# Performance work log

Measured on AMD Instinct MI355X. Metric: run time of the kernel, lower is better.

## Reference

```python
import jax, jax.numpy as jnp
import numpy as np
from jax import lax

RATIOS = (0.5, 1.0, 2.0)
SCALES = (8, 16, 32)
BASE = 16
STRIDE = 16
N_PRE = 6000
N_POST = 300      # post-NMS proposals kept
NMS_THRESH = 0.7
MIN_SIZE = 16.0


def _anchor_base():
    x = y = BASE / 2.0
    ab = np.zeros((len(RATIOS) * len(SCALES), 4), np.float32)
    for i, r in enumerate(RATIOS):
        for j, s in enumerate(SCALES):
            h = BASE * s * np.sqrt(r)
            w = BASE * s * np.sqrt(1.0 / r)
            k = i * len(SCALES) + j
            ab[k] = [y - h / 2, x - w / 2, y + h / 2, x + w / 2]
    return ab


def _anchors(h, w):
    ab = _anchor_base()
    sy = np.arange(0, h * STRIDE, STRIDE)
    sx = np.arange(0, w * STRIDE, STRIDE)
    sx, sy = np.meshgrid(sx, sy)
    shift = np.stack((sy.ravel(), sx.ravel(), sy.ravel(), sx.ravel()), axis=1)
    # [K, A, 4] -> [K*A, 4], row-major over (y, x) pixels matching NHWC flatten
    return (ab[None, :, :] + shift[:, None, :]).reshape(-1, 4).astype(np.float32)


def _conv(x, w, b, pad):
    y = lax.conv_general_dilated(x, w, (1, 1), ((pad, pad), (pad, pad)),
                                 dimension_numbers=('NCHW', 'OIHW', 'NCHW'))
    return y + b[None, :, None, None]


def _loc2bbox(anchor, loc):
    h = anchor[:, 2] - anchor[:, 0]
    w = anchor[:, 3] - anchor[:, 1]
    cy = anchor[:, 0] + 0.5 * h
    cx = anchor[:, 1] + 0.5 * w
    dy, dx, dh, dw = loc[:, 0], loc[:, 1], loc[:, 2], loc[:, 3]
    ncy = dy * h + cy
    ncx = dx * w + cx
    nh = jnp.exp(dh) * h
    nw = jnp.exp(dw) * w
    return jnp.stack([ncy - 0.5 * nh, ncx - 0.5 * nw, ncy + 0.5 * nh, ncx + 0.5 * nw], axis=1)


def _iou(b):
    tl = jnp.maximum(b[:, None, :2], b[None, :, :2])
    br = jnp.minimum(b[:, None, 2:], b[None, :, 2:])
    wh = jnp.clip(br - tl, 0.0)
    inter = wh[..., 0] * wh[..., 1]
    area = (b[:, 2] - b[:, 0]) * (b[:, 3] - b[:, 1])
    return inter / (area[:, None] + area[None, :] - inter + 1e-9)


def _nms_keep(iou):
    # greedy NMS over score-sorted boxes: suppress later boxes overlapping kept earlier ones
    n = iou.shape[0]
    idx = jnp.arange(n)
    def step(keep, i):
        sup = (iou[i] > NMS_THRESH) & (idx > i) & keep[i]
        return keep & (~sup), None
    keep, _ = lax.scan(step, jnp.ones((n,), dtype=bool), idx)
    return keep


def _proposal(loc, fg, anchor, img_h, img_w, scale=1.0):
    boxes = _loc2bbox(anchor, loc)
    boxes = jnp.stack([jnp.clip(boxes[:, 0], 0.0, img_h),
                       jnp.clip(boxes[:, 1], 0.0, img_w),
                       jnp.clip(boxes[:, 2], 0.0, img_h),
                       jnp.clip(boxes[:, 3], 0.0, img_w)], axis=1)
    hs = boxes[:, 2] - boxes[:, 0]
    ws = boxes[:, 3] - boxes[:, 1]
    ms = MIN_SIZE * scale
    score = jnp.where((hs >= ms) & (ws >= ms), fg, -jnp.inf)
    top, idx = lax.top_k(score, N_PRE)
    bk = boxes[idx]                                    # [N_PRE, 4]
    keep = _nms_keep(_iou(lax.stop_gradient(bk)))      # selection is non-differentiable
    fs = jnp.where(keep, top, -jnp.inf)
    _, o2 = lax.top_k(fs, N_POST)
    return bk[o2]                                      # [N_POST, 4]


def setup_inputs() -> dict:
    key = jax.random.key(0)
    ks = jax.random.split(key, 4)
    C, H, W = 512, 50, 76
    return {
        "feature": jax.random.normal(ks[0], (1, C, H, W), jnp.float32),
        "conv1_w": jax.random.normal(ks[1], (512, C, 3, 3), jnp.float32) * 0.01,
        "conv1_b": jnp.zeros((512,), jnp.float32),
        "score_w": jax.random.normal(ks[2], (18, 512, 1, 1), jnp.float32) * 0.01,
        "score_b": jnp.zeros((18,), jnp.float32),
        "loc_w": jax.random.normal(ks[3], (36, 512, 1, 1), jnp.float32) * 0.01,
        "loc_b": jnp.zeros((36,), jnp.float32),
        "img_h": 800,
        "img_w": 1216,
    }


def reference(feature, conv1_w, conv1_b, score_w, score_b, loc_w, loc_b, img_h, img_w):
    _, c, h, w = feature.shape
    A = 9
    anchor = jnp.asarray(_anchors(h, w))
    x = jax.nn.relu(_conv(feature, conv1_w, conv1_b, 1))
    locs = _conv(x, loc_w, loc_b, 0)
    rpn_locs = locs.transpose(0, 2, 3, 1).reshape(1, -1, 4)
    sc = _conv(x, score_w, score_b, 0).transpose(0, 2, 3, 1)   # [1, h, w, 2A]
    sm = jax.nn.softmax(sc.reshape(1, h, w, A, 2), axis=-1)
    fg = sm[..., 1].reshape(-1)
    rpn_scores = sc.reshape(1, -1, 2)
    rois = _proposal(rpn_locs[0], fg, anchor, float(img_h), float(img_w), scale=1.0)
    return rpn_locs, rpn_scores, rois, anchor
```

## Files before the change

### kernel.cpp

```cpp
#include <hip/hip_runtime.h>

#define HH 50
#define WW2 76
#define NPIX 3800
#define CIN 512
#define NANCH 34200
#define NPRE 6000
#define NPOST 300
#define WPR 94

typedef unsigned long long u64;
typedef unsigned int u32;

__device__ __forceinline__ int PADL(int i) { return i + (i >> 4); }

template <bool DOW>
__global__ __launch_bounds__(256) void rpn_wtrans(const float* __restrict__ wgt,
                                                  float* __restrict__ wt,
                                                  const float* __restrict__ sw,
                                                  const float* __restrict__ lw,
                                                  float* __restrict__ wt2,
                                                  u32* __restrict__ hist,
                                                  u32* __restrict__ info) {
    __shared__ float tile[32][33];
    const int bx = blockIdx.x;
    const int by = blockIdx.y;
    const int t  = threadIdx.x;
    const int tx = t & 31, ty = t >> 5;
    int gid = (by * 144 + bx) * 256 + t;
    if (gid < 65536) hist[gid] = 0u;
    else if (gid < 65552) info[gid - 65536] = 0u;
    if (gid < 32768) {
        int c = gid >> 6, n = gid & 63;
        float v = 0.f;
        if (n < 18) v = sw[n * 512 + c];
        else if (n < 54) v = lw[(n - 18) * 512 + c];
        wt2[((c >> 2) * 64 + n) * 4 + (c & 3)] = v;
    }
    if (!DOW) return;
#pragma unroll
    for (int r = 0; r < 32; r += 8) {
        int ko = by * 32 + ty + r;
        tile[ty + r][tx] = wgt[(size_t)ko * 4608 + bx * 32 + tx];
    }
    __syncthreads();
#pragma unroll
    for (int r = 0; r < 32; r += 8) {
        int cit = bx * 32 + ty + r;
        wt[(size_t)cit * 512 + by * 32 + tx] = tile[tx][ty + r];
    }
}

template <bool USEWT>
__global__ __launch_bounds__(256, 4) void rpn_conv1(
    const float* __restrict__ feat, const float* __restrict__ wsrc,
    float* __restrict__ Xp, int cin_blk) {
    const int yb = blockIdx.x;
    const int kg = blockIdx.y;
    const int cz = blockIdx.z;
    const int t  = threadIdx.x;
    const int kp = t & 31;
    const int ty = t >> 5;
    const int row  = ty >> 2;
    const int xseg = ty & 3;
    const int x0 = xseg * 20;
    __shared__ float in_l[1408];
    __shared__ float w_l[2304];

    const int y0 = yb * 2 - 1;
    int inSrc[6]; u32 inValid = 0, inPad = 0;
#pragma unroll
    for (int k = 0; k < 6; ++k) {
        int q = t + k * 256;
        int c = q / 336, rem = q - c * 336;
        int r = rem / 84, xx = rem - r * 84;
        int gy = y0 + r, gx = xx - 1;
        bool inb = q < 1344;
        bool ok = inb && ((unsigned)gy < 50u) && ((unsigned)gx < 76u);
        inSrc[k] = c * NPIX + gy * 76 + gx;
        if (ok) inValid |= (1u << k);
        else if (inb) inPad |= (1u << k);
    }
#pragma unroll
    for (int k = 0; k < 6; ++k)
        if ((inPad >> k) & 1) in_l[t + k * 256] = 0.f;

    const float* wb;
    int wOffA = 0;
    int wSrc[9];
    if (USEWT) {
        wb = wsrc + (size_t)(cz * cin_blk) * 9 * 512 + kg * 64;
        wOffA = 8 * t - 7 * (t & 63);
    } else {
        wb = wsrc + (size_t)(kg * 64) * 4608 + (size_t)(cz * cin_blk) * 9;
#pragma unroll
        for (int k = 0; k < 9; ++k) {
            int q = t + k * 256;
            int c = q / 576, r2 = q - c * 576;
            int tap = r2 >> 6, ko = r2 & 63;
            wSrc[k] = ko * 4608 + c * 9 + tap;
        }
    }

    const float* fb = feat + (size_t)(cz * cin_blk) * NPIX;
    float acc0[20], acc1[20];
#pragma unroll
    for (int p = 0; p < 20; ++p) { acc0[p] = 0.f; acc1[p] = 0.f; }

    const int niter = cin_blk >> 2;
#pragma unroll 1
    for (int it = 0; it < niter; ++it) {
        __syncthreads();
#pragma unroll
        for (int k = 0; k < 6; ++k)
            if ((inValid >> k) & 1) in_l[t + k * 256] = fb[inSrc[k]];
        if (USEWT) {
#pragma unroll
            for (int k = 0; k < 9; ++k)
                w_l[t + k * 256] = wb[wOffA + k * 2048];
        } else {
#pragma unroll
            for (int k = 0; k < 9; ++k)
                w_l[t + k * 256] = wb[wSrc[k]];
        }
        __syncthreads();
#pragma unroll 1
        for (int c = 0; c < 4; ++c) {
            const float* ir0 = &in_l[(c * 4 + row) * 84 + x0];
            const float* wl  = &w_l[c * 576 + 2 * kp];
#pragma unroll
            for (int r = 0; r < 3; ++r) {
                const float* ir = ir0 + r * 84;
                float win[22];
#pragma unroll
                for (int w = 0; w < 22; ++w) win[w] = ir[w];
                float w00 = wl[(r * 3 + 0) * 64],     w01 = wl[(r * 3 + 1) * 64],     w02 = wl[(r * 3 + 2) * 64];
                float w10 = wl[(r * 3 + 0) * 64 + 1], w11 = wl[(r * 3 + 1) * 64 + 1], w12 = wl[(r * 3 + 2) * 64 + 1];
#pragma unroll
                for (int p = 0; p < 20; ++p) {
                    acc0[p] = fmaf(w00, win[p],     acc0[p]);
                    acc0[p] = fmaf(w01, win[p + 1], acc0[p]);
                    acc0[p] = fmaf(w02, win[p + 2], acc0[p]);
                    acc1[p] = fmaf(w10, win[p],     acc1[p]);
                    acc1[p] = fmaf(w11, win[p + 1], acc1[p]);
                    acc1[p] = fmaf(w12, win[p + 2], acc1[p]);
                }
            }
        }
        fb += 4 * NPIX;
        wb += USEWT ? 4 * 9 * 512 : 36;
    }

    const int k0 = kg * 64 + 2 * kp;
    const int y = yb * 2 + row;
    float* d0 = Xp + ((size_t)cz * 512 + k0) * NPIX + y * 76 + x0;
#pragma unroll
    for (int p = 0; p < 20; p += 2) {
        if (x0 + p + 1 < 76) {
            *reinterpret_cast<float2*>(d0 + p)        = make_float2(acc0[p], acc0[p + 1]);
            *reinterpret_cast<float2*>(d0 + NPIX + p) = make_float2(acc1[p], acc1[p + 1]);
        }
    }
}

__global__ __launch_bounds__(256) void rpn_combine(
    const float* __restrict__ Xp, const float* __restrict__ bias,
    float* __restrict__ Xt, int nz) {
    const int p0 = blockIdx.x * 256;
    const int c0 = blockIdx.y * 16;
    const int t  = threadIdx.x;
    __shared__ float s[16][257];
    const int p = p0 + t;
#pragma unroll 4
    for (int i = 0; i < 16; ++i) {
        float v = 0.f;
        if (p < NPIX) {
            size_t base = (size_t)(c0 + i) * NPIX + p;
            float a = bias[c0 + i];
            for (int z = 0; z < nz; ++z) a += Xp[(size_t)z * 512 * NPIX + base];
            v = fmaxf(a, 0.f);
        }
        s[i][t] = v;
    }
    __syncthreads();
    const int cs = (t & 3) * 4;
    const int pr = t >> 2;
#pragma unroll
    for (int q = 0; q < 4; ++q) {
        int p2 = p0 + pr + q * 64;
        if (p2 < NPIX) {
            int pi = pr + q * 64;
            float4 v = make_float4(s[cs][pi], s[cs + 1][pi], s[cs + 2][pi], s[cs + 3][pi]);
            *reinterpret_cast<float4*>(&Xt[(size_t)p2 * 512 + c0 + cs]) = v;
        }
    }
}

__global__ __launch_bounds__(64) void rpn_head(
    const float* __restrict__ Xt, const float* __restrict__ wt2,
    const float* __restrict__ sb, const float* __restrict__ lb,
    const int* __restrict__ ihp, const int* __restrict__ iwp,
    float* __restrict__ out, float* __restrict__ boxes,
    u32* __restrict__ keys, u32* __restrict__ hist) {
    const int p0 = blockIdx.x * 8;
    const int t  = threadIdx.x;
    __shared__ __align__(16) float xs[8 * 512];
    __shared__ float ovl[8][64];
    const float4* src = reinterpret_cast<const float4*>(Xt + (size_t)p0 * 512);
    float4* dst = reinterpret_cast<float4*>(xs);
#pragma unroll
    for (int i = 0; i < 16; ++i) dst[t + i * 64] = src[t + i * 64];
    __syncthreads();
    float acc[8];
    {
        float b = (t < 18) ? sb[t] : ((t < 54) ? lb[t - 18] : 0.f);
#pragma unroll
        for (int px = 0; px < 8; ++px) acc[px] = b;
    }
    const float4* wv = reinterpret_cast<const float4*>(wt2) + t;
#pragma unroll 4
    for (int c4 = 0; c4 < 128; ++c4) {
        float4 w = wv[c4 * 64];
#pragma unroll
        for (int px = 0; px < 8; ++px) {
            float4 x = *reinterpret_cast<const float4*>(xs + px * 512 + c4 * 4);
            acc[px] = fmaf(w.x, x.x, acc[px]);
            acc[px] = fmaf(w.y, x.y, acc[px]);
            acc[px] = fmaf(w.z, x.z, acc[px]);
            acc[px] = fmaf(w.w, x.w, acc[px]);
        }
    }
#pragma unroll
    for (int px = 0; px < 8; ++px) ovl[px][t] = acc[px];
    __syncthreads();
    const float ch = (float)(*ihp), cw = (float)(*iwp);
#pragma unroll
    for (int pass = 0; pass < 2; ++pass) {
        int a, px;
        bool act;
        if (pass == 0) { act = (t < 63); px = t / 9; a = t - px * 9; }
        else           { act = (t < 9);  px = 7;     a = t; }
        if (act) {
            const int p = p0 + px;
            const float* ov = ovl[px];
            const float s0 = ov[2 * a], s1 = ov[2 * a + 1];
            const float dy = ov[18 + 4 * a], dx = ov[18 + 4 * a + 1];
            const float dh = ov[18 + 4 * a + 2], dw = ov[18 + 4 * a + 3];
            const int yy = p / WW2, xx = p % WW2;
            const int ai = p * 9 + a;
            *reinterpret_cast<float4*>(out + ai * 4) = make_float4(dy, dx, dh, dw);
            *reinterpret_cast<float2*>(out + 136800 + ai * 2) = make_float2(s0, s1);
            double r  = (a < 3) ? 0.5 : (a < 6) ? 1.0 : 2.0;
            int m3 = a % 3;
            double s2 = (m3 == 0) ? 8.0 : (m3 == 1) ? 16.0 : 32.0;
            double hd = (16.0 * s2) * sqrt(r);
            double wd = (16.0 * s2) * sqrt(1.0 / r);
            float ay1 = (float)(8.0 - hd * 0.5), ax1 = (float)(8.0 - wd * 0.5);
            float ay2 = (float)(8.0 + hd * 0.5), ax2 = (float)(8.0 + wd * 0.5);
            float fy = (float)(yy * 16), fx = (float)(xx * 16);
            float A0 = ay1 + fy, A1 = ax1 + fx, A2 = ay2 + fy, A3 = ax2 + fx;
            *reinterpret_cast<float4*>(out + 206400 + ai * 4) = make_float4(A0, A1, A2, A3);
            float ah = __fsub_rn(A2, A0), aw = __fsub_rn(A3, A1);
            float cy = __fadd_rn(A0, __fmul_rn(0.5f, ah));
            float cx = __fadd_rn(A1, __fmul_rn(0.5f, aw));
            float ncy = __fadd_rn(__fmul_rn(dy, ah), cy);
            float ncx = __fadd_rn(__fmul_rn(dx, aw), cx);
            float nh = __fmul_rn(expf(dh), ah);
            float nw = __fmul_rn(expf(dw), aw);
            float b0 = __fsub_rn(ncy, __fmul_rn(0.5f, nh));
            float b1 = __fsub_rn(ncx, __fmul_rn(0.5f, nw));
            float b2 = __fadd_rn(ncy, __fmul_rn(0.5f, nh));
            float b3 = __fadd_rn(ncx, __fmul_rn(0.5f, nw));
            b0 = fminf(fmaxf(b0, 0.f), ch); b2 = fminf(fmaxf(b2, 0.f), ch);
            b1 = fminf(fmaxf(b1, 0.f), cw); b3 = fminf(fmaxf(b3, 0.f), cw);
            float hs = __fsub_rn(b2, b0), wsz = __fsub_rn(b3, b1);
            float m = fmaxf(s0, s1);
            float e0 = expf(__fsub_rn(s0, m)), e1 = expf(__fsub_rn(s1, m));
            float fg = __fdiv_rn(e1, __fadd_rn(e0, e1));
            float score = (hs >= 16.f && wsz >= 16.f) ? fg : -__builtin_inff();
            *reinterpret_cast<float4*>(boxes + ai * 4) = make_float4(b0, b1, b2, b3);
            u32 kb = __float_as_uint(score);
            kb = (kb & 0x80000000u) ? ~kb : (kb | 0x80000000u);
            keys[ai] = kb;
            atomicAdd(&hist[kb >> 16], 1u);
        }
    }
}

__global__ __launch_bounds__(1024) void rpn_topk(const u32* __restrict__ hist,
                                                 const u32* __restrict__ keys,
                                                 const float* __restrict__ boxes,
                                                 float* __restrict__ bk) {
    __shared__ u64 s[8704];
    __shared__ u32 part[256], h2[256];
    __shared__ int segs;
    __shared__ u32 Tsh, cnt;
    const int t = threadIdx.x;
    if (t == 0) cnt = 0u;
    u32* tmp = (u32*)s;
    {
        u32 sum = 0;
        const u32* hp = hist + t * 64;
#pragma unroll 8
        for (int b = 0; b < 64; ++b) sum += hp[b];
        tmp[t] = sum;
    }
    __syncthreads();
    u32 p4 = 0;
    if (t < 256) p4 = tmp[4 * t] + tmp[4 * t + 1] + tmp[4 * t + 2] + tmp[4 * t + 3];
    __syncthreads();
    if (t < 256) part[t] = p4;
    __syncthreads();
    for (int off = 1; off < 256; off <<= 1) {
        u32 v = 0, add = 0;
        if (t < 256) { v = part[t]; add = (t + off < 256) ? part[t + off] : 0u; }
        __syncthreads();
        if (t < 256) part[t] = v + add;
        __syncthreads();
    }
    if (t < 256) {
        u32 suf  = part[t];
        u32 sufn = (t < 255) ? part[t + 1] : 0u;
        if (suf >= NPRE && sufn < NPRE) segs = t;
    }
    __syncthreads();
    const int seg = segs;
    const u32 above = (seg < 255) ? part[seg + 1] : 0u;
    if (t < 256) h2[t] = hist[seg * 256 + t];
    __syncthreads();
    for (int off = 1; off < 256; off <<= 1) {
        u32 v = 0, add = 0;
        if (t < 256) { v = h2[t]; add = (t + off < 256) ? h2[t + off] : 0u; }
        __syncthreads();
        if (t < 256) h2[t] = v + add;
        __syncthreads();
    }
    if (t < 256) {
        u32 tot  = above + h2[t];
        u32 totn = above + ((t < 255) ? h2[t + 1] : 0u);
        if (tot >= NPRE && totn < NPRE) Tsh = (u32)(seg * 256 + t);
    }
    __syncthreads();
    const u32 T = Tsh;
    const int lane = t & 63;
    for (int base = 0; base < NANCH; base += 1024) {
        int idx = base + t;
        u32 k = (idx < NANCH) ? keys[idx] : 0u;
        bool sel = (idx < NANCH) && ((k >> 16) >= T);
        u64 ball = __ballot(sel);
        u32 wbase = 0;
        if (lane == 0 && ball) wbase = atomicAdd(&cnt, (u32)__popcll(ball));
        wbase = __shfl(wbase, 0);
        if (sel) {
            u32 pos = wbase + (u32)__popcll(ball & ((1ull << lane) - 1ull));
            if (pos < 8192) s[PADL((int)pos)] = ((u64)k << 32) | (u64)(0xFFFFFFFFu - (u32)idx);
        }
    }
    __syncthreads();
    {
        int n = (int)cnt; if (n > 8192) n = 8192;
        for (int i = t; i < 8192; i += 1024)
            if (i >= n) s[PADL(i)] = 0ull;
    }
    __syncthreads();
    for (int k = 2; k <= 8192; k <<= 1) {
        for (int j = k >> 1; j > 0; j >>= 1) {
#pragma unroll 4
            for (int z = 0; z < 4; ++z) {
                int pi = t + z * 1024;
                int p1 = ((pi & ~(j - 1)) << 1) | (pi & (j - 1));
                int p2 = p1 | j;
                bool desc = ((p1 & k) == 0);
                u64 A = s[PADL(p1)], B = s[PADL(p2)];
                if (desc ? (A < B) : (A > B)) { s[PADL(p1)] = B; s[PADL(p2)] = A; }
            }
            __syncthreads();
        }
    }
    for (int i = t; i < NPRE; i += 1024) {
        u32 oi = 0xFFFFFFFFu - (u32)(s[PADL(i)] & 0xFFFFFFFFull);
        if (oi >= NANCH) oi = 0;
        reinterpret_cast<float4*>(bk)[i] = reinterpret_cast<const float4*>(boxes)[oi];
    }
}

__global__ __launch_bounds__(64) void rpn_iou(const float* __restrict__ bk,
                                              u64* __restrict__ mask) {
    const int t = threadIdx.x;
    const int bj = blockIdx.x, bi = blockIdx.y;
    const int j0 = bj * 64;
    const int i = bi * 64 + t;
    if (j0 + 63 <= bi * 64) {
        if (i < NPRE) mask[(size_t)i * WPR + bj] = 0ull;
        return;
    }
    __shared__ float4 jb[64];
    jb[t] = (j0 + t < NPRE) ? reinterpret_cast<const float4*>(bk)[j0 + t]
                            : make_float4(0.f, 0.f, 0.f, 0.f);
    __syncthreads();
    if (i >= NPRE) return;
    float4 b = reinterpret_cast<const float4*>(bk)[i];
    float areai = __fmul_rn(__fsub_rn(b.z, b.x), __fsub_rn(b.w, b.y));
    u64 bits = 0ull;
    for (int jj = 0; jj < 64; ++jj) {
        int j = j0 + jj;
        if (j <= i || j >= NPRE) continue;
        float4 c = jb[jj];
        float ty = fmaxf(b.x, c.x), tx = fmaxf(b.y, c.y);
        float by = fminf(b.z, c.z), bx2 = fminf(b.w, c.w);
        float ih = fmaxf(__fsub_rn(by, ty), 0.f);
        float iw = fmaxf(__fsub_rn(bx2, tx), 0.f);
        float inter = __fmul_rn(ih, iw);
        float areaj = __fmul_rn(__fsub_rn(c.z, c.x), __fsub_rn(c.w, c.y));
        float denom = __fadd_rn(__fsub_rn(__fadd_rn(areai, areaj), inter), 1e-9f);
        float iou = __fdiv_rn(inter, denom);
        if (iou > 0.7f) bits |= (1ull << jj);
    }
    mask[(size_t)i * WPR + bj] = bits;
}

__global__ __launch_bounds__(64) void rpn_nms(const u64* __restrict__ mask,
                                              const float* __restrict__ bk,
                                              float* __restrict__ rois) {
    const int lane = threadIdx.x;
    u64 rem0 = 0ull, rem1 = 0ull, curW = 0ull;
    __shared__ unsigned short klist[304];
    int kcnt = 0;
    u64 pm0[16], pm1[16], pmg[16];
#pragma unroll
    for (int u = 0; u < 16; ++u) {
        pm0[u] = mask[(size_t)u * WPR + lane];
        pm1[u] = (lane < 30) ? mask[(size_t)u * WPR + 64 + lane] : 0ull;
        pmg[u] = mask[(size_t)u * WPR + 0];
    }
    bool done = false;
    for (int base = 0; base < NPRE && !done; base += 16) {
        if ((base & 63) == 0) {
            int w = base >> 6;
            curW = (w < 64) ? __shfl(rem0, w) : __shfl(rem1, w - 64);
        }
#pragma unroll
        for (int u = 0; u < 16; ++u) {
            const int i = base + u;
            u64 m0 = pm0[u], m1 = pm1[u], mg = pmg[u];
            const int ni = i + 16;
            pm0[u] = mask[(size_t)ni * WPR + lane];
            pm1[u] = (lane < 30) ? mask[(size_t)ni * WPR + 64 + lane] : 0ull;
            pmg[u] = mask[(size_t)ni * WPR + (ni >> 6)];
            if (((curW >> (i & 63)) & 1ull) == 0ull) {
                rem0 |= m0;
                rem1 |= m1;
                curW |= mg;
                if (lane == 0 && kcnt < 304) klist[kcnt] = (unsigned short)i;
                ++kcnt;
                if (kcnt >= NPOST) { done = true; break; }
            }
        }
    }
    __syncthreads();
    const int nk = kcnt < NPOST ? kcnt : NPOST;
    for (int r = lane; r < nk; r += 64) {
        int bi = klist[r];
        reinterpret_cast<float4*>(rois)[r] = reinterpret_cast<const float4*>(bk)[bi];
    }
    if (kcnt < NPOST) {
        int pos = kcnt;
        for (int i = 0; i < NPRE && pos < NPOST; ++i) {
            int w = i >> 6;
            u64 wv = (w < 64) ? __shfl(rem0, w) : __shfl(rem1, w - 64);
            if ((wv >> (i & 63)) & 1ull) {
                if (lane < 4) rois[pos * 4 + lane] = bk[i * 4 + lane];
                ++pos;
            }
        }
    }
}

extern "C" void kernel_launch(void* const* d_in, const int* in_sizes, int n_in,
                              void* d_out, int out_size, void* d_ws, size_t ws_size,
                              hipStream_t stream) {
    (void)in_sizes; (void)n_in; (void)out_size;
    const float* feat = (const float*)d_in[0];
    const float* w1   = (const float*)d_in[1];
    const float* b1   = (const float*)d_in[2];
    const float* sw   = (const float*)d_in[3];
    const float* sb   = (const float*)d_in[4];
    const float* lw   = (const float*)d_in[5];
    const float* lb   = (const float*)d_in[6];
    const int*   ih   = (const int*)d_in[7];
    const int*   iw   = (const int*)d_in[8];
    float* out = (float*)d_out;

    const size_t WT_B    = 9437184;
    const size_t WT2_B   = 131072;
    const size_t XT_B    = 7782400;
    const size_t REST_B  = WT2_B + 547200 + 136800 + 262144 + 64 + 96000 + 4528128;
    const size_t SLICE_B = (size_t)512 * NPIX * 4;
    int nz; bool usewt;
    if      (ws_size >= 8 * SLICE_B + WT_B + XT_B + REST_B) { nz = 8; usewt = true; }
    else if (ws_size >= 4 * SLICE_B + WT_B + XT_B + REST_B) { nz = 4; usewt = true; }
    else if (ws_size >= 2 * SLICE_B + WT_B + XT_B + REST_B) { nz = 2; usewt = true; }
    else                                                    { nz = 2; usewt = false; }

    char* p = (char*)d_ws;
    float* Xp = (float*)p;           p += (size_t)nz * SLICE_B;
    float* wt = nullptr;
    if (usewt) { wt = (float*)p;     p += WT_B; }
    float* Xt     = (float*)p;       p += XT_B;
    float* wt2    = (float*)p;       p += WT2_B;
    float* boxes  = (float*)p;       p += 547200;
    u32*   keys   = (u32*)p;         p += 136800;
    u32*   hist   = (u32*)p;         p += 262144;
    u32*   info   = (u32*)p;         p += 64;
    float* bk     = (float*)p;       p += 96000;
    u64*   mask   = (u64*)p;

    const int cin_blk = 512 / nz;

    if (usewt) {
        rpn_wtrans<true><<<dim3(144, 16), 256, 0, stream>>>(w1, wt, sw, lw, wt2, hist, info);
        rpn_conv1<true><<<dim3(25, 8, nz), 256, 0, stream>>>(feat, wt, Xp, cin_blk);
    } else {
        rpn_wtrans<false><<<dim3(144, 16), 256, 0, stream>>>(w1, nullptr, sw, lw, wt2, hist, info);
        rpn_conv1<false><<<dim3(25, 8, nz), 256, 0, stream>>>(feat, w1, Xp, cin_blk);
    }
    rpn_combine<<<dim3(15, 32), 256, 0, stream>>>(Xp, b1, Xt, nz);
    rpn_head<<<475, 64, 0, stream>>>(Xt, wt2, sb, lb, ih, iw, out, boxes, keys, hist);
    rpn_topk<<<1, 1024, 0, stream>>>(hist, keys, boxes, bk);
    rpn_iou<<<dim3(WPR, WPR), 64, 0, stream>>>(bk, mask);
    rpn_nms<<<1, 64, 0, stream>>>(mask, bk, out + 205200);
}
```

Before: 656.4 us.

## Retile conv1 to 4 outputs x 4 rows, write NHWC, fuse combine into head

The conv1 kernel now computes 4 output channels per thread over 4 output rows per block (19-pixel segments), which raises register reuse of the input window across more channels. Partial results are written directly in pixel-major (NHWC) layout with float4 stores. The separate combine kernel is removed, and the split-K partial sums plus bias and ReLU are now reduced inside the head kernel as it loads its tile. This saves one launch and one full intermediate round trip, at the cost of higher register pressure (occupancy hint lowered to 2) and strided per-thread output stores.

Measured after the change: 623.9 us. 5.0% less time.

```diff
diff --git a/kernel.cpp b/kernel.cpp
--- a/kernel.cpp
+++ b/kernel.cpp
@@ -52,37 +52,37 @@
 }
 
 template <bool USEWT>
-__global__ __launch_bounds__(256, 4) void rpn_conv1(
+__global__ __launch_bounds__(256, 2) void rpn_conv1(
     const float* __restrict__ feat, const float* __restrict__ wsrc,
-    float* __restrict__ Xp, int cin_blk) {
+    float* __restrict__ Xpt, int cin_blk) {
     const int yb = blockIdx.x;
     const int kg = blockIdx.y;
     const int cz = blockIdx.z;
     const int t  = threadIdx.x;
-    const int kp = t & 31;
-    const int ty = t >> 5;
+    const int kp = t & 15;
+    const int ty = t >> 4;
     const int row  = ty >> 2;
     const int xseg = ty & 3;
-    const int x0 = xseg * 20;
-    __shared__ float in_l[1408];
+    const int x0 = xseg * 19;
+    __shared__ float in_l[2048];
     __shared__ float w_l[2304];
 
-    const int y0 = yb * 2 - 1;
-    int inSrc[6]; u32 inValid = 0, inPad = 0;
-#pragma unroll
-    for (int k = 0; k < 6; ++k) {
+    const int y0 = yb * 4 - 1;
+    int inSrc[8]; u32 inValid = 0, inPad = 0;
+#pragma unroll
+    for (int k = 0; k < 8; ++k) {
         int q = t + k * 256;
-        int c = q / 336, rem = q - c * 336;
+        int c = q / 504, rem = q - c * 504;
         int r = rem / 84, xx = rem - r * 84;
         int gy = y0 + r, gx = xx - 1;
-        bool inb = q < 1344;
+        bool inb = q < 2016;
         bool ok = inb && ((unsigned)gy < 50u) && ((unsigned)gx < 76u);
         inSrc[k] = c * NPIX + gy * 76 + gx;
         if (ok) inValid |= (1u << k);
         else if (inb) inPad |= (1u << k);
     }
 #pragma unroll
-    for (int k = 0; k < 6; ++k)
+    for (int k = 0; k < 8; ++k)
         if ((inPad >> k) & 1) in_l[t + k * 256] = 0.f;
 
     const float* wb;
@@ -103,16 +103,18 @@
     }
 
     const float* fb = feat + (size_t)(cz * cin_blk) * NPIX;
-    float acc0[20], acc1[20];
-#pragma unroll
-    for (int p = 0; p < 20; ++p) { acc0[p] = 0.f; acc1[p] = 0.f; }
+    float acc[4][19];
+#pragma unroll
+    for (int o = 0; o < 4; ++o)
+#pragma unroll
+        for (int p = 0; p < 19; ++p) acc[o][p] = 0.f;
 
     const int niter = cin_blk >> 2;
 #pragma unroll 1
     for (int it = 0; it < niter; ++it) {
         __syncthreads();
 #pragma unroll
-        for (int k = 0; k < 6; ++k)
+        for (int k = 0; k < 8; ++k)
             if ((inValid >> k) & 1) in_l[t + k * 256] = fb[inSrc[k]];
         if (USEWT) {
 #pragma unroll
@@ -126,24 +128,29 @@
         __syncthreads();
 #pragma unroll 1
         for (int c = 0; c < 4; ++c) {
-            const float* ir0 = &in_l[(c * 4 + row) * 84 + x0];
-            const float* wl  = &w_l[c * 576 + 2 * kp];
+            const float* ir0 = &in_l[(c * 6 + row) * 84 + x0];
+            const float* wl  = &w_l[c * 576 + 4 * kp];
 #pragma unroll
             for (int r = 0; r < 3; ++r) {
                 const float* ir = ir0 + r * 84;
-                float win[22];
-#pragma unroll
-                for (int w = 0; w < 22; ++w) win[w] = ir[w];
-                float w00 = wl[(r * 3 + 0) * 64],     w01 = wl[(r * 3 + 1) * 64],     w02 = wl[(r * 3 + 2) * 64];
-                float w10 = wl[(r * 3 + 0) * 64 + 1], w11 = wl[(r * 3 + 1) * 64 + 1], w12 = wl[(r * 3 + 2) * 64 + 1];
-#pragma unroll
-                for (int p = 0; p < 20; ++p) {
-                    acc0[p] = fmaf(w00, win[p],     acc0[p]);
-                    acc0[p] = fmaf(w01, win[p + 1], acc0[p]);
-                    acc0[p] = fmaf(w02, win[p + 2], acc0[p]);
-                    acc1[p] = fmaf(w10, win[p],     acc1[p]);
-                    acc1[p] = fmaf(w11, win[p + 1], acc1[p]);
-                    acc1[p] = fmaf(w12, win[p + 2], acc1[p]);
+                float win[21];
+#pragma unroll
+                for (int w = 0; w < 21; ++w) win[w] = ir[w];
+                float wv[4][3];
+#pragma unroll
+                for (int tp = 0; tp < 3; ++tp) {
+                    const float* wr = wl + (r * 3 + tp) * 64;
+#pragma unroll
+                    for (int o = 0; o < 4; ++o) wv[o][tp] = wr[o];
+                }
+#pragma unroll
+                for (int p = 0; p < 19; ++p) {
+#pragma unroll
+                    for (int o = 0; o < 4; ++o) {
+                        acc[o][p] = fmaf(wv[o][0], win[p],     acc[o][p]);
+                        acc[o][p] = fmaf(wv[o][1], win[p + 1], acc[o][p]);
+                        acc[o][p] = fmaf(wv[o][2], win[p + 2], acc[o][p]);
+                    }
                 }
             }
         }
@@ -151,65 +158,43 @@
         wb += USEWT ? 4 * 9 * 512 : 36;
     }
 
-    const int k0 = kg * 64 + 2 * kp;
-    const int y = yb * 2 + row;
-    float* d0 = Xp + ((size_t)cz * 512 + k0) * NPIX + y * 76 + x0;
-#pragma unroll
-    for (int p = 0; p < 20; p += 2) {
-        if (x0 + p + 1 < 76) {
-            *reinterpret_cast<float2*>(d0 + p)        = make_float2(acc0[p], acc0[p + 1]);
-            *reinterpret_cast<float2*>(d0 + NPIX + p) = make_float2(acc1[p], acc1[p + 1]);
-        }
-    }
-}
-
-__global__ __launch_bounds__(256) void rpn_combine(
-    const float* __restrict__ Xp, const float* __restrict__ bias,
-    float* __restrict__ Xt, int nz) {
-    const int p0 = blockIdx.x * 256;
-    const int c0 = blockIdx.y * 16;
-    const int t  = threadIdx.x;
-    __shared__ float s[16][257];
-    const int p = p0 + t;
-#pragma unroll 4
-    for (int i = 0; i < 16; ++i) {
-        float v = 0.f;
-        if (p < NPIX) {
-            size_t base = (size_t)(c0 + i) * NPIX + p;
-            float a = bias[c0 + i];
-            for (int z = 0; z < nz; ++z) a += Xp[(size_t)z * 512 * NPIX + base];
-            v = fmaxf(a, 0.f);
-        }
-        s[i][t] = v;
-    }
-    __syncthreads();
-    const int cs = (t & 3) * 4;
-    const int pr = t >> 2;
-#pragma unroll
-    for (int q = 0; q < 4; ++q) {
-        int p2 = p0 + pr + q * 64;
-        if (p2 < NPIX) {
-            int pi = pr + q * 64;
-            float4 v = make_float4(s[cs][pi], s[cs + 1][pi], s[cs + 2][pi], s[cs + 3][pi]);
-            *reinterpret_cast<float4*>(&Xt[(size_t)p2 * 512 + c0 + cs]) = v;
-        }
+    const int k0 = kg * 64 + 4 * kp;
+    const int y = yb * 4 + row;
+    if (y < 50) {
+        float* d0 = Xpt + ((size_t)cz * NPIX + y * 76 + x0) * 512 + k0;
+#pragma unroll
+        for (int p = 0; p < 19; ++p)
+            *reinterpret_cast<float4*>(d0 + (size_t)p * 512) =
+                make_float4(acc[0][p], acc[1][p], acc[2][p], acc[3][p]);
     }
 }
 
 __global__ __launch_bounds__(64) void rpn_head(
-    const float* __restrict__ Xt, const float* __restrict__ wt2,
+    const float* __restrict__ Xpt, const float* __restrict__ wt2,
+    const float* __restrict__ b1,
     const float* __restrict__ sb, const float* __restrict__ lb,
     const int* __restrict__ ihp, const int* __restrict__ iwp,
     float* __restrict__ out, float* __restrict__ boxes,
-    u32* __restrict__ keys, u32* __restrict__ hist) {
+    u32* __restrict__ keys, u32* __restrict__ hist, int nz) {
     const int p0 = blockIdx.x * 8;
     const int t  = threadIdx.x;
     __shared__ __align__(16) float xs[8 * 512];
     __shared__ float ovl[8][64];
-    const float4* src = reinterpret_cast<const float4*>(Xt + (size_t)p0 * 512);
     float4* dst = reinterpret_cast<float4*>(xs);
 #pragma unroll
-    for (int i = 0; i < 16; ++i) dst[t + i * 64] = src[t + i * 64];
+    for (int i = 0; i < 16; ++i) {
+        int idx = t + i * 64;
+        int px = idx >> 7, cc = idx & 127;
+        float4 v = *reinterpret_cast<const float4*>(b1 + cc * 4);
+        const float* src = Xpt + ((size_t)(p0 + px)) * 512 + cc * 4;
+        for (int z = 0; z < nz; ++z) {
+            float4 x = *reinterpret_cast<const float4*>(src + (size_t)z * NPIX * 512);
+            v.x += x.x; v.y += x.y; v.z += x.z; v.w += x.w;
+        }
+        v.x = fmaxf(v.x, 0.f); v.y = fmaxf(v.y, 0.f);
+        v.z = fmaxf(v.z, 0.f); v.w = fmaxf(v.w, 0.f);
+        dst[idx] = v;
+    }
     __syncthreads();
     float acc[8];
     {
@@ -268,17 +253,17 @@
             float nh = __fmul_rn(expf(dh), ah);
             float nw = __fmul_rn(expf(dw), aw);
             float b0 = __fsub_rn(ncy, __fmul_rn(0.5f, nh));
-            float b1 = __fsub_rn(ncx, __fmul_rn(0.5f, nw));
+            float b1v = __fsub_rn(ncx, __fmul_rn(0.5f, nw));
             float b2 = __fadd_rn(ncy, __fmul_rn(0.5f, nh));
             float b3 = __fadd_rn(ncx, __fmul_rn(0.5f, nw));
             b0 = fminf(fmaxf(b0, 0.f), ch); b2 = fminf(fmaxf(b2, 0.f), ch);
-            b1 = fminf(fmaxf(b1, 0.f), cw); b3 = fminf(fmaxf(b3, 0.f), cw);
-            float hs = __fsub_rn(b2, b0), wsz = __fsub_rn(b3, b1);
+            b1v = fminf(fmaxf(b1v, 0.f), cw); b3 = fminf(fmaxf(b3, 0.f), cw);
+            float hs = __fsub_rn(b2, b0), wsz = __fsub_rn(b3, b1v);
             float m = fmaxf(s0, s1);
             float e0 = expf(__fsub_rn(s0, m)), e1 = expf(__fsub_rn(s1, m));
             float fg = __fdiv_rn(e1, __fadd_rn(e0, e1));
             float score = (hs >= 16.f && wsz >= 16.f) ? fg : -__builtin_inff();
-            *reinterpret_cast<float4*>(boxes + ai * 4) = make_float4(b0, b1, b2, b3);
+            *reinterpret_cast<float4*>(boxes + ai * 4) = make_float4(b0, b1v, b2, b3);
             u32 kb = __float_as_uint(score);
             kb = (kb & 0x80000000u) ? ~kb : (kb | 0x80000000u);
             keys[ai] = kb;
@@ -493,20 +478,18 @@
 
     const size_t WT_B    = 9437184;
     const size_t WT2_B   = 131072;
-    const size_t XT_B    = 7782400;
     const size_t REST_B  = WT2_B + 547200 + 136800 + 262144 + 64 + 96000 + 4528128;
     const size_t SLICE_B = (size_t)512 * NPIX * 4;
     int nz; bool usewt;
-    if      (ws_size >= 8 * SLICE_B + WT_B + XT_B + REST_B) { nz = 8; usewt = true; }
-    else if (ws_size >= 4 * SLICE_B + WT_B + XT_B + REST_B) { nz = 4; usewt = true; }
-    else if (ws_size >= 2 * SLICE_B + WT_B + XT_B + REST_B) { nz = 2; usewt = true; }
-    else                                                    { nz = 2; usewt = false; }
+    if      (ws_size >= 8 * SLICE_B + WT_B + REST_B) { nz = 8; usewt = true; }
+    else if (ws_size >= 4 * SLICE_B + WT_B + REST_B) { nz = 4; usewt = true; }
+    else if (ws_size >= 2 * SLICE_B + WT_B + REST_B) { nz = 2; usewt = true; }
+    else                                             { nz = 2; usewt = false; }
 
     char* p = (char*)d_ws;
-    float* Xp = (float*)p;           p += (size_t)nz * SLICE_B;
+    float* Xpt = (float*)p;          p += (size_t)nz * SLICE_B;
     float* wt = nullptr;
     if (usewt) { wt = (float*)p;     p += WT_B; }
-    float* Xt     = (float*)p;       p += XT_B;
     float* wt2    = (float*)p;       p += WT2_B;
     float* boxes  = (float*)p;       p += 547200;
     u32*   keys   = (u32*)p;         p += 136800;
@@ -519,13 +502,12 @@
 
     if (usewt) {
         rpn_wtrans<true><<<dim3(144, 16), 256, 0, stream>>>(w1, wt, sw, lw, wt2, hist, info);
-        rpn_conv1<true><<<dim3(25, 8, nz), 256, 0, stream>>>(feat, wt, Xp, cin_blk);
+        rpn_conv1<true><<<dim3(13, 8, nz), 256, 0, stream>>>(feat, wt, Xpt, cin_blk);
     } else {
         rpn_wtrans<false><<<dim3(144, 16), 256, 0, stream>>>(w1, nullptr, sw, lw, wt2, hist, info);
-        rpn_conv1<false><<<dim3(25, 8, nz), 256, 0, stream>>>(feat, w1, Xp, cin_blk);
-    }
-    rpn_combine<<<dim3(15, 32), 256, 0, stream>>>(Xp, b1, Xt, nz);
-    rpn_head<<<475, 64, 0, stream>>>(Xt, wt2, sb, lb, ih, iw, out, boxes, keys, hist);
+        rpn_conv1<false><<<dim3(13, 8, nz), 256, 0, stream>>>(feat, w1, Xpt, cin_blk);
+    }
+    rpn_head<<<475, 64, 0, stream>>>(Xpt, wt2, b1, sb, lb, ih, iw, out, boxes, keys, hist, nz);
     rpn_topk<<<1, 1024, 0, stream>>>(hist, keys, boxes, bk);
     rpn_iou<<<dim3(WPR, WPR), 64, 0, stream>>>(bk, mask);
     rpn_nms<<<1, 64, 0, stream>>>(mask, bk, out + 205200);
```
